# Performance work log

Measured on AMD Instinct MI355X. Metric: run time of the kernel, lower is better.

## Reference

```python
import jax, jax.numpy as jnp
import numpy as np

N = 100000
E = 1600000
IN_DIM = 1024
H_DIM = 16
DIM2 = H_DIM * 8  # 128


def _xavier(key, shape):
    fan_in, fan_out = shape[-2], shape[-1]
    lim = (6.0 / (fan_in + fan_out)) ** 0.5
    return jax.random.uniform(key, shape, jnp.float32, -lim, lim)


def setup_inputs() -> dict:
    key = jax.random.key(0)
    ks = jax.random.split(key, 10)
    x = jax.random.normal(ks[0], (N, IN_DIM), jnp.float32)
    edge_index = jax.random.randint(ks[1], (2, E), 0, N)
    perm = jax.random.permutation(ks[2], N)
    W1 = _xavier(ks[3], (IN_DIM, DIM2)); b1 = jnp.zeros((DIM2,), jnp.float32)
    W2 = _xavier(ks[4], (DIM2, DIM2)); b2 = jnp.zeros((DIM2,), jnp.float32)
    W3 = _xavier(ks[5], (DIM2, H_DIM)); b3 = jnp.zeros((H_DIM,), jnp.float32)
    Wdo = _xavier(ks[6], (1, DIM2, DIM2)); bdo = jnp.zeros((1,), jnp.float32)
    Wdh = _xavier(ks[7], (1, H_DIM, H_DIM)); bdh = jnp.zeros((1,), jnp.float32)
    return dict(x=x, W1=W1, b1=b1, W2=W2, b2=b2, W3=W3, b3=b3,
                Wdo=Wdo, bdo=bdo, Wdh=Wdh, bdh=bdh,
                edge_index=edge_index, perm=perm)


def _graph_conv(x, W, b, src, dst, norm_src, norm_dst):
    # DGL GraphConv, norm='both': D_dst^{-1/2} A D_src^{-1/2} X W + b
    h = (x * norm_src[:, None]) @ W          # mult W first (in >= out)
    agg = jax.ops.segment_sum(h[src], dst, num_segments=N)
    return agg * norm_dst[:, None] + b


def _l2norm(x):
    n = jnp.sqrt(jnp.sum(x * x, axis=1, keepdims=True))
    return x / jnp.maximum(n, 1e-12)


def _bilinear(a, c, W, b):
    # nn.Bilinear(n_h, n_h, 1): out[n,k] = a[n] @ W[k] @ c[n] + b[k]
    return jnp.einsum('nd,kde,ne->nk', a, W, c) + b


def reference(x, W1, b1, W2, b2, W3, b3, Wdo, bdo, Wdh, bdh, edge_index, perm):
    src, dst = edge_index[0], edge_index[1]
    ones = jnp.ones((E,), jnp.float32)
    deg_out = jnp.maximum(jax.ops.segment_sum(ones, src, num_segments=N), 1.0)
    deg_in = jnp.maximum(jax.ops.segment_sum(ones, dst, num_segments=N), 1.0)
    ns, nd = deg_out ** -0.5, deg_in ** -0.5

    def encode(xin):
        o = _graph_conv(xin, W1, b1, src, dst, ns, nd)
        o = _graph_conv(o, W2, b2, src, dst, ns, nd) + o
        h = _graph_conv(o, W3, b3, src, dst, ns, nd)
        emb_o = jax.nn.relu(o)
        g_o = jax.nn.sigmoid(_l2norm(emb_o))
        emb_h = jax.nn.relu(h)
        g_h = jax.nn.sigmoid(_l2norm(emb_h))
        return h, emb_o, g_o, emb_h, g_h

    h, emb_o, g_o, emb_h, g_h = encode(x)
    h_a, emb_oa, g_oa, emb_ha, g_ha = encode(x[perm])

    def disc(c, h_pl, h_mi, W, b):
        return jnp.concatenate([_bilinear(h_pl, c, W, b), _bilinear(h_mi, c, W, b)], axis=1)

    ret_o = disc(g_o, emb_o, emb_oa, Wdo, bdo)
    ret_oa = disc(g_oa, emb_oa, emb_o, Wdo, bdo)
    ret_h = disc(g_h, emb_h, emb_ha, Wdh, bdh)
    ret_ha = disc(g_ha, emb_ha, emb_h, Wdh, bdh)
    return (h, ret_o, ret_h, ret_oa, ret_ha)
```

## Files before the change

kernel.cpp:

```cpp
#include <hip/hip_runtime.h>
#include <math.h>

#define NN 100000
#define EE 1600000
#define SCB 98

typedef __attribute__((ext_vector_type(8))) short bf16x8;
typedef __attribute__((ext_vector_type(4))) short bf16x4;
typedef __attribute__((ext_vector_type(4))) float f32x4;

__device__ __forceinline__ unsigned short f2bf(float x){
  union { float f; unsigned u; } v; v.f = x;
  unsigned r = v.u + 0x7FFFu + ((v.u >> 16) & 1u);
  return (unsigned short)(r >> 16);
}
__device__ __forceinline__ float bf2f(unsigned short h){
  union { unsigned u; float f; } v; v.u = ((unsigned)h) << 16; return v.f;
}
__device__ __forceinline__ float sigm(float x){ return 1.0f/(1.0f+__expf(-x)); }

__device__ __forceinline__ void gload16(const unsigned short* g, unsigned short* l){
  __builtin_amdgcn_global_load_lds(
    (const __attribute__((address_space(1))) void*)g,
    (__attribute__((address_space(3))) void*)l, 16, 0, 0);
}
template<int N>
__device__ __forceinline__ void waitvm(){
  if constexpr (N==0) asm volatile("s_waitcnt vmcnt(0)" ::: "memory");
  else if constexpr (N==2) asm volatile("s_waitcnt vmcnt(2)" ::: "memory");
  else if constexpr (N==4) asm volatile("s_waitcnt vmcnt(4)" ::: "memory");
  else if constexpr (N==8) asm volatile("s_waitcnt vmcnt(8)" ::: "memory");
}
__device__ __forceinline__ void membar(){ asm volatile("" ::: "memory"); }

__global__ __launch_bounds__(256) void k_deg_wcvt(const int* __restrict__ src, const int* __restrict__ dst,
                      int* __restrict__ dout, int* __restrict__ din,
                      const float* __restrict__ W1, const float* __restrict__ W2,
                      const float* __restrict__ Wdo, const float* __restrict__ W3,
                      unsigned short* __restrict__ W1T, unsigned short* __restrict__ W2T,
                      unsigned short* __restrict__ WdoB, unsigned short* __restrict__ W3c){
  int b = blockIdx.x;
  if (b < EE/256){
    int e = b*256 + threadIdx.x;
    atomicAdd(&dout[src[e]],1); atomicAdd(&din[dst[e]],1);
  } else {
    int i = (b - EE/256)*256 + threadIdx.x;
    if (i < 131072){
      int c = i>>13, s = i&8191;
      int col = s>>6, p = (s>>3)&7, e2 = s&7;
      int k = c*64 + 8*(p ^ (col&7)) + e2;
      W1T[i] = f2bf(W1[(size_t)k*128 + col]);
    } else if (i < 147456){
      int j = i-131072;
      int c = j>>13, s = j&8191;
      int col = s>>6, p = (s>>3)&7, e2 = s&7;
      int k = c*64 + 8*(p ^ (col&7)) + e2;
      W2T[j] = f2bf(W2[(size_t)k*128 + col]);
    } else if (i < 163840){
      int j = i-147456;
      int c = j>>13, s = j&8191;
      int col = s>>6, p = (s>>3)&7, e2 = s&7;
      int k = c*64 + 8*(p ^ (col&7)) + e2;
      WdoB[j] = f2bf(Wdo[(size_t)col*128 + k]);
    } else if (i < 165888){
      int j = i-163840;
      int col = j>>7, k = j&127;
      W3c[j] = f2bf(W3[(size_t)k*16 + col]);
    }
  }
}

__global__ __launch_bounds__(1024) void k_scan1(const int* __restrict__ din, int* __restrict__ chunk,
                        int* __restrict__ bsum){
  __shared__ int wsum[16];
  int t = threadIdx.x, lane = t & 63, w = t >> 6;
  int i = blockIdx.x*1024 + t;
  int v = (i < NN) ? din[i] : 0;
  int x = v;
  #pragma unroll
  for (int off=1; off<64; off<<=1){
    int y = __shfl_up(x, off);
    if (lane>=off) x += y;
  }
  if (lane==63) wsum[w] = x;
  __syncthreads();
  int pre = 0;
  #pragma unroll
  for (int j=0;j<16;j++) if (j<w) pre += wsum[j];
  int incl = x + pre;
  if (i < NN) chunk[i] = incl;
  if (t == 1023) bsum[blockIdx.x] = incl;
}

__global__ __launch_bounds__(128) void k_scan2(const int* __restrict__ bsum, int* __restrict__ bpre,
                       int* __restrict__ row_ptr){
  __shared__ int w0tot;
  int t = threadIdx.x, lane = t & 63, w = t >> 6;
  int v = (t < SCB) ? bsum[t] : 0;
  int x = v;
  #pragma unroll
  for (int off=1; off<64; off<<=1){
    int y = __shfl_up(x, off);
    if (lane>=off) x += y;
  }
  if (w==0 && lane==63) w0tot = x;
  __syncthreads();
  int incl = x + (w ? w0tot : 0);
  if (t < SCB) bpre[t] = incl - v;
  if (t == 0) row_ptr[0] = 0;
}

__global__ __launch_bounds__(256) void k_scan3(const int* __restrict__ din, const int* __restrict__ chunk,
                       const int* __restrict__ bpre, const int* __restrict__ dout,
                       const int* __restrict__ perm,
                       int* __restrict__ row_ptr, int* __restrict__ cursor,
                       float* __restrict__ ns, float* __restrict__ nd, int* __restrict__ inv){
  int i = blockIdx.x*256 + threadIdx.x;
  if (i < NN){
    int d = din[i];
    int val = chunk[i] + bpre[i>>10];
    row_ptr[i+1] = val;
    cursor[i] = val - d;
    ns[i] = rsqrtf((float)max(dout[i],1));
    nd[i] = rsqrtf((float)max(d,1));
    inv[perm[i]] = i;
  }
}

__global__ __launch_bounds__(256) void k_fill(const int* __restrict__ src, const int* __restrict__ dst,
                       int* __restrict__ cursor, int* __restrict__ col){
  int e = blockIdx.x*256+threadIdx.x;
  if (e<EE){ int pos = atomicAdd(&cursor[dst[e]],1); col[pos] = src[e]; }
}

struct ARF { float4 a, b; };
struct ARU { bf16x8 a; };
__device__ __forceinline__ void aload(ARF& r, const float* p){
  r.a = *(const float4*)p; r.b = *(const float4*)(p+4);
}
__device__ __forceinline__ void aload(ARU& r, const unsigned short* p){
  r.a = *(const bf16x8*)p;
}
template<int IM>
__device__ __forceinline__ bf16x8 aconv(const ARF& r, float rs){
  float av[8] = {r.a.x,r.a.y,r.a.z,r.a.w,r.b.x,r.b.y,r.b.z,r.b.w};
  if constexpr (IM==1){
    #pragma unroll
    for (int i=0;i<8;i++) av[i] = sigm(fmaxf(av[i],0.0f)*rs);
  }
  bf16x8 o;
  #pragma unroll
  for (int i=0;i<8;i++) o[i] = (short)f2bf(av[i]);
  return o;
}
template<int IM>
__device__ __forceinline__ bf16x8 aconv(const ARU& r, float rs){
  if constexpr (IM==0) return r.a;
  else {
    bf16x8 o;
    #pragma unroll
    for (int i=0;i<8;i++){
      float v = sigm(fmaxf(bf2f((unsigned short)r.a[i]),0.0f)*rs);
      o[i] = (short)f2bf(v);
    }
    return o;
  }
}
__device__ __forceinline__ bf16x8 araw(const ARU& r){ return r.a; }
__device__ __forceinline__ bf16x8 araw(const ARF& r){
  bf16x8 o;
  float av[8] = {r.a.x,r.a.y,r.a.z,r.a.w,r.b.x,r.b.y,r.b.z,r.b.w};
  #pragma unroll
  for (int i=0;i<8;i++) o[i] = (short)f2bf(av[i]);
  return o;
}
template<typename T> struct ARofT;
template<> struct ARofT<float>{ using type = ARF; };
template<> struct ARofT<unsigned short>{ using type = ARU; };

template<int KDIM, int IN_MODE, int OUT_MODE, typename AT>
__global__ __launch_bounds__(256,4) void k_gemmA(
    const AT* __restrict__ A, const unsigned short* __restrict__ Wc,
    unsigned short* __restrict__ out0,
    const float* __restrict__ scale, const int* __restrict__ inv,
    const float* __restrict__ rn, int nrows,
    float* __restrict__ ro, float* __restrict__ roa,
    const unsigned short* __restrict__ W3c, const float* __restrict__ ns2,
    unsigned short* __restrict__ th)
{
  constexpr int NC = KDIM/64;
  constexpr int APC = (sizeof(AT)==4) ? 4 : 2;
  constexpr int BSSZ = 2*128*64 + (OUT_MODE==3 ? 2048 : 0);
  __shared__ __align__(16) unsigned short Bs[BSSZ];
  unsigned short* W3s = &Bs[16384];
  int t = threadIdx.x, wave = t>>6, lane = t&63;
  int row0 = blockIdx.x*64;
  int arow = row0 + wave*16 + (lane&15);
  int kof = (lane>>4)*8;
  int arow_c = min(arow, nrows-1);
  const AT* ap = A + (size_t)arow_c*KDIM + kof;
  float rscale = 1.0f;
  if constexpr (IN_MODE==1) rscale = rn[arow_c];

  unsigned short* b0 = &Bs[0];
  unsigned short* b1 = &Bs[128*64];
  const unsigned short* bcur = b0; unsigned short* bnxt = b1;

  f32x4 acc[8] = {};
  f32x4 acc2 = {};
  typename ARofT<AT>::type A0a{},A0b{},A1a{},A1b{},A2a{},A2b{};

  if constexpr (OUT_MODE==3){
    int wc = t>>4, wsl = t&15;
    bf16x8 v = *(const bf16x8*)(W3c + wc*128 + wsl*8);
    *(bf16x8*)&W3s[wc*128 + ((wsl ^ (wc&7))<<3)] = v;
  }
  membar();
  {
    unsigned short* lb = b0 + wave*2048;
    const unsigned short* gb = Wc + wave*2048 + lane*8;
    #pragma unroll
    for (int q=0;q<4;q++) gload16(gb + q*512, lb + q*512);
  }
  membar();
  aload(A0a, ap); aload(A0b, ap+32);
  if (NC>1){ aload(A1a, ap+64); aload(A1b, ap+96); }
  waitvm<2*APC>();
  asm volatile("s_waitcnt lgkmcnt(0)" ::: "memory");
  __builtin_amdgcn_s_barrier();
  __builtin_amdgcn_sched_barrier(0);

  int slot0 = lane>>4;
  int c = lane & 15;
  #pragma unroll
  for (int cc=0; cc<NC; ++cc){
    if (cc+1 < NC){
      unsigned short* lb = bnxt + wave*2048;
      const unsigned short* gb = Wc + (size_t)(cc+1)*8192 + wave*2048 + lane*8;
      #pragma unroll
      for (int q=0;q<4;q++) gload16(gb + q*512, lb + q*512);
    }
    membar();
    if (cc+2 < NC){
      aload(A2a, ap + (cc+2)*64);
      aload(A2b, ap + (cc+2)*64 + 32);
    }
    membar();
    {
      bf16x8 af = aconv<IN_MODE>(A0a, rscale);
      #pragma unroll
      for (int j=0;j<8;j++){
        int cj = j*16 + c;
        bf16x8 b = *(const bf16x8*)&bcur[cj*64 + ((slot0 ^ (cj&7))<<3)];
        acc[j] = __builtin_amdgcn_mfma_f32_16x16x32_bf16(af, b, acc[j], 0, 0, 0);
      }
      if constexpr (OUT_MODE==3){
        int sl = cc*8 + slot0;
        bf16x8 b = *(const bf16x8*)&W3s[c*128 + ((sl ^ (c&7))<<3)];
        acc2 = __builtin_amdgcn_mfma_f32_16x16x32_bf16(araw(A0a), b, acc2, 0, 0, 0);
      }
    }
    {
      bf16x8 af = aconv<IN_MODE>(A0b, rscale);
      #pragma unroll
      for (int j=0;j<8;j++){
        int cj = j*16 + c;
        bf16x8 b = *(const bf16x8*)&bcur[cj*64 + (((slot0+4) ^ (cj&7))<<3)];
        acc[j] = __builtin_amdgcn_mfma_f32_16x16x32_bf16(af, b, acc[j], 0, 0, 0);
      }
      if constexpr (OUT_MODE==3){
        int sl = cc*8 + 4 + slot0;
        bf16x8 b = *(const bf16x8*)&W3s[c*128 + ((sl ^ (c&7))<<3)];
        acc2 = __builtin_amdgcn_mfma_f32_16x16x32_bf16(araw(A0b), b, acc2, 0, 0, 0);
      }
    }
    if (cc+1 < NC){
      if (cc+2 < NC) waitvm<APC>(); else waitvm<0>();
      __builtin_amdgcn_s_barrier();
      __builtin_amdgcn_sched_barrier(0);
      const unsigned short* tmp = bcur; bcur = bnxt; bnxt = (unsigned short*)tmp;
    }
    A0a=A1a; A0b=A1b; A1a=A2a; A1b=A2b;
  }

  if constexpr (OUT_MODE==3){
    #pragma unroll
    for (int r=0;r<4;r++){
      int row = row0 + wave*16 + (lane>>4)*4 + r;
      int sidx = row>=NN ? row-NN : row;
      float v = acc2[r]*ns2[sidx];
      size_t tof = row<NN ? (size_t)row*32 + c : (size_t)(row-NN)*32 + 16 + c;
      th[tof] = f2bf(v);
    }
    __syncthreads();
    unsigned short* Os = &Bs[0];
    unsigned short* Oo = &Bs[8192];
    for (int p=t; p<2048; p+=256){
      int r = (p>>4)&63, seg = p&15;
      int row = row0 + r;
      int srcrow = (p<1024) ? row : (row<NN ? row+NN : row-NN);
      unsigned short* dst = (p<1024) ? Os : Oo;
      *(bf16x8*)&dst[r*128 + ((seg ^ (r&7))<<3)] = *(const bf16x8*)&A[(size_t)srcrow*128 + seg*8];
    }
    __syncthreads();
    float bb = scale[0];
    #pragma unroll
    for (int r=0;r<4;r++){
      int lr = wave*16 + (lane>>4)*4 + r;
      float dsame=0.f, doth=0.f;
      #pragma unroll
      for (int j=0;j<8;j++){
        float v = acc[j][r];
        int colj = j*16 + c;
        int idx = lr*128 + (((colj>>3) ^ (lr&7))<<3) + (colj&7);
        dsame += fmaxf(bf2f(Os[idx]),0.f)*v;
        doth  += fmaxf(bf2f(Oo[idx]),0.f)*v;
      }
      #pragma unroll
      for (int off=1; off<16; off<<=1){
        dsame += __shfl_xor(dsame, off);
        doth  += __shfl_xor(doth, off);
      }
      if (c==0){
        int row = row0 + lr;
        if (row < NN){
          ro[(size_t)row*2+0] = dsame + bb;
          ro[(size_t)row*2+1] = doth + bb;
        } else {
          int m = row - NN;
          roa[(size_t)m*2+0] = dsame + bb;
          roa[(size_t)m*2+1] = doth + bb;
        }
      }
    }
  } else {
    int rbase = row0 + wave*16 + (lane>>4)*4;
    #pragma unroll
    for (int j=0;j<8;j++){
      int colx = j*16 + c;
      #pragma unroll
      for (int r=0;r<4;r++){
        int row = rbase + r;
        if (row < nrows){
          float v = acc[j][r];
          if constexpr (OUT_MODE==0){
            out0[(size_t)row*256 + colx] = f2bf(v * scale[row]);
            int ir = inv[row];
            out0[(size_t)ir*256 + 128 + colx] = f2bf(v * scale[ir]);
          } else {
            int sidx = row >= NN ? row - NN : row;
            size_t zof = row < NN ? (size_t)row*256 + colx : (size_t)(row-NN)*256 + 128 + colx;
            out0[zof] = f2bf(v * scale[sidx]);
          }
        }
      }
    }
  }
}

template<bool RESID>
__global__ __launch_bounds__(256) void k_agg128(
  const unsigned short* __restrict__ z,
  const int* __restrict__ row_ptr, const int* __restrict__ col,
  const float* __restrict__ nd, const float* __restrict__ bias,
  unsigned short* __restrict__ ob, float* __restrict__ rn)
{
  int wave = threadIdx.x>>6, lane = threadIdx.x&63;
  int row = blockIdx.x*4 + wave;
  if (row >= NN) return;
  int s = row_ptr[row], e = row_ptr[row+1];
  int es = lane>>5;
  int half = (lane>>4)&1;
  int c8 = (lane&15)*8;
  size_t lof = (size_t)half*128 + c8;
  float acc[8] = {};
  int i = s + es;
  int c0 = (i < e) ? col[i] : -1;
  int c1 = (i+2 < e) ? col[i+2] : -1;
  bf16x8 u0 = {}, u1 = {};
  if (c0 >= 0) u0 = *(const bf16x8*)(z + (size_t)c0*256 + lof);
  if (c1 >= 0) u1 = *(const bf16x8*)(z + (size_t)c1*256 + lof);
  int d0 = (i+4 < e) ? col[i+4] : -1;
  int d1 = (i+6 < e) ? col[i+6] : -1;
  bf16x8 v0 = {}, v1 = {};
  if (d0 >= 0) v0 = *(const bf16x8*)(z + (size_t)d0*256 + lof);
  if (d1 >= 0) v1 = *(const bf16x8*)(z + (size_t)d1*256 + lof);
  while (c0 >= 0){
    int n0 = (i+8 < e) ? col[i+8] : -1;
    int n1 = (i+10 < e) ? col[i+10] : -1;
    bf16x8 w0 = {}, w1 = {};
    if (n0 >= 0) w0 = *(const bf16x8*)(z + (size_t)n0*256 + lof);
    if (n1 >= 0) w1 = *(const bf16x8*)(z + (size_t)n1*256 + lof);
    #pragma unroll
    for (int j=0;j<8;j++) acc[j] += bf2f((unsigned short)u0[j]);
    if (c1 >= 0){
      #pragma unroll
      for (int j=0;j<8;j++) acc[j] += bf2f((unsigned short)u1[j]);
    }
    c0=d0; c1=d1; u0=v0; u1=v1;
    d0=n0; d1=n1; v0=w0; v1=w1;
    i += 4;
  }
  #pragma unroll
  for (int j=0;j<8;j++) acc[j] += __shfl_down(acc[j], 32);
  if (lane < 32){
    float ndr = nd[row];
    size_t oof = half ? (size_t)(NN+row)*128 + c8 : (size_t)row*128 + c8;
    float ra[8];
    #pragma unroll
    for (int j=0;j<8;j++) ra[j] = acc[j]*ndr + bias[c8+j];
    if constexpr (RESID){
      bf16x8 pv = *(const bf16x8*)(ob + oof);
      #pragma unroll
      for (int j=0;j<8;j++) ra[j] += bf2f((unsigned short)pv[j]);
    }
    bf16x8 wv;
    #pragma unroll
    for (int j=0;j<8;j++) wv[j] = (short)f2bf(ra[j]);
    *(bf16x8*)(ob + oof) = wv;
    if constexpr (RESID){
      float sa = 0.f;
      #pragma unroll
      for (int j=0;j<8;j++){ float x1 = fmaxf(ra[j],0.f); sa += x1*x1; }
      sa += __shfl_down(sa, 8);
      sa += __shfl_down(sa, 4);
      sa += __shfl_down(sa, 2);
      sa += __shfl_down(sa, 1);
      if ((lane&15)==0) rn[half ? NN+row : row] = 1.0f/fmaxf(sqrtf(sa),1e-12f);
    }
  }
}

__global__ __launch_bounds__(256) void k_agg16(
  const unsigned short* __restrict__ th,
  const int* __restrict__ row_ptr, const int* __restrict__ col,
  const float* __restrict__ nd, const float* __restrict__ b3,
  const float* __restrict__ Wdh, const float* __restrict__ bdh,
  float* __restrict__ hout, float* __restrict__ rh, float* __restrict__ rha)
{
  __shared__ float Ws[256];
  __shared__ float hbuf[4][32];
  __shared__ float gbuf[4][32];
  int t = threadIdx.x;
  Ws[t] = Wdh[t];
  __syncthreads();
  int wave = t>>6, lane = t&63;
  int row = blockIdx.x*4 + wave;
  if (row >= NN) return;
  int s = row_ptr[row], e = row_ptr[row+1];
  int es = lane>>3, l8 = lane&7;
  float a4[4] = {};
  int i = s + es;
  int sc0 = (i<e)? col[i] : -1;
  int sc1 = (i+8<e)? col[i+8] : -1;
  bf16x4 u0 = {}, u1 = {};
  if (sc0 >= 0) u0 = *(const bf16x4*)(th + (size_t)sc0*32 + l8*4);
  if (sc1 >= 0) u1 = *(const bf16x4*)(th + (size_t)sc1*32 + l8*4);
  while (sc0 >= 0){
    int ni = i + 16;
    int nsc0 = (ni<e)? col[ni] : -1;
    int nsc1 = (ni+8<e)? col[ni+8] : -1;
    bf16x4 v0 = {}, v1 = {};
    if (nsc0 >= 0) v0 = *(const bf16x4*)(th + (size_t)nsc0*32 + l8*4);
    if (nsc1 >= 0) v1 = *(const bf16x4*)(th + (size_t)nsc1*32 + l8*4);
    #pragma unroll
    for (int j=0;j<4;j++) a4[j] += bf2f((unsigned short)u0[j]);
    if (sc1 >= 0){
      #pragma unroll
      for (int j=0;j<4;j++) a4[j] += bf2f((unsigned short)u1[j]);
    }
    u0 = v0; u1 = v1; sc0 = nsc0; sc1 = nsc1; i = ni;
  }
  #pragma unroll
  for (int j=0;j<4;j++){
    a4[j] += __shfl_down(a4[j], 32);
    a4[j] += __shfl_down(a4[j], 16);
    a4[j] += __shfl_down(a4[j], 8);
  }
  if (lane < 8){
    float ndr = nd[row];
    int half = l8>>2, c0 = (l8&3)*4;
    float4 r;
    r.x = a4[0]*ndr + b3[c0+0];
    r.y = a4[1]*ndr + b3[c0+1];
    r.z = a4[2]*ndr + b3[c0+2];
    r.w = a4[3]*ndr + b3[c0+3];
    if (half==0) *(float4*)&hout[(size_t)row*16 + c0] = r;
    int hb = half*16 + c0;
    hbuf[wave][hb+0]=r.x; hbuf[wave][hb+1]=r.y; hbuf[wave][hb+2]=r.z; hbuf[wave][hb+3]=r.w;
  }
  if (lane < 16){
    int d = lane;
    float e1v = fmaxf(hbuf[wave][d],    0.f);
    float e2v = fmaxf(hbuf[wave][16+d], 0.f);
    float s1 = e1v*e1v, s2 = e2v*e2v;
    #pragma unroll
    for (int off=1; off<16; off<<=1){
      s1 += __shfl_xor(s1, off);
      s2 += __shfl_xor(s2, off);
    }
    float r1 = 1.0f/fmaxf(sqrtf(s1),1e-12f);
    float r2 = 1.0f/fmaxf(sqrtf(s2),1e-12f);
    gbuf[wave][d]    = sigm(e1v*r1);
    gbuf[wave][16+d] = sigm(e2v*r2);
    float vh1=0.f, vh2=0.f;
    #pragma unroll
    for (int e2i=0;e2i<16;e2i++){
      float w = Ws[d*16+e2i];
      vh1 += w*gbuf[wave][e2i];
      vh2 += w*gbuf[wave][16+e2i];
    }
    float q00 = e1v*vh1, q01 = e2v*vh1, q10 = e2v*vh2, q11 = e1v*vh2;
    #pragma unroll
    for (int off=1; off<16; off<<=1){
      q00 += __shfl_xor(q00, off);
      q01 += __shfl_xor(q01, off);
      q10 += __shfl_xor(q10, off);
      q11 += __shfl_xor(q11, off);
    }
    if (lane==0){
      float bb = bdh[0];
      rh [(size_t)row*2+0]=q00+bb; rh [(size_t)row*2+1]=q01+bb;
      rha[(size_t)row*2+0]=q10+bb; rha[(size_t)row*2+1]=q11+bb;
    }
  }
}

extern "C" void kernel_launch(void* const* d_in, const int* in_sizes, int n_in,
                              void* d_out, int out_size, void* d_ws, size_t ws_size,
                              hipStream_t stream){
  const float* x   = (const float*)d_in[0];
  const float* W1  = (const float*)d_in[1];
  const float* b1  = (const float*)d_in[2];
  const float* W2  = (const float*)d_in[3];
  const float* b2  = (const float*)d_in[4];
  const float* W3  = (const float*)d_in[5];
  const float* b3  = (const float*)d_in[6];
  const float* Wdo = (const float*)d_in[7];
  const float* bdo = (const float*)d_in[8];
  const float* Wdh = (const float*)d_in[9];
  const float* bdh = (const float*)d_in[10];
  const int* ei    = (const int*)d_in[11];
  const int* perm  = (const int*)d_in[12];
  const int* esrc = ei;
  const int* edst = ei + EE;

  char* ws = (char*)d_ws;
  size_t off = 0;
  auto alloc = [&](size_t bytes)->void*{ void* p = ws + off; off += (bytes + 255) & ~(size_t)255; return p; };
  unsigned short* z  = (unsigned short*)alloc((size_t)NN*256*2);
  unsigned short* ob = (unsigned short*)alloc((size_t)2*NN*128*2);
  unsigned short* th = (unsigned short*)alloc((size_t)NN*32*2);
  int* deg = (int*)alloc((size_t)2*NN*4);
  int* dout_ = deg; int* din_ = deg + NN;
  float* ns = (float*)alloc((size_t)NN*4);
  float* nd = (float*)alloc((size_t)NN*4);
  int* inv  = (int*)alloc((size_t)NN*4);
  float* rn = (float*)alloc((size_t)2*NN*4);
  int* cursor = (int*)alloc((size_t)NN*4);
  int* row_ptr = (int*)alloc((size_t)(NN+1)*4);
  int* colx = (int*)alloc((size_t)EE*4);
  int* chunk = (int*)alloc((size_t)NN*4);
  int* bsum = (int*)alloc((size_t)SCB*4);
  int* bpre = (int*)alloc((size_t)SCB*4);
  unsigned short* W1T = (unsigned short*)alloc((size_t)1024*128*2);
  unsigned short* W2T = (unsigned short*)alloc((size_t)128*128*2);
  unsigned short* WdoB = (unsigned short*)alloc((size_t)128*128*2);
  unsigned short* W3c = (unsigned short*)alloc((size_t)16*128*2);

  float* out_h   = (float*)d_out;
  float* out_ro  = out_h  + (size_t)NN*16;
  float* out_rh  = out_ro + (size_t)NN*2;
  float* out_roa = out_rh + (size_t)NN*2;
  float* out_rha = out_roa+ (size_t)NN*2;

  hipMemsetAsync(deg, 0, (size_t)2*NN*4, stream);
  k_deg_wcvt<<<EE/256 + 648, 256, 0, stream>>>(esrc, edst, dout_, din_,
                                               W1, W2, Wdo, W3, W1T, W2T, WdoB, W3c);
  k_scan1<<<SCB, 1024, 0, stream>>>(din_, chunk, bsum);
  k_scan2<<<1, 128, 0, stream>>>(bsum, bpre, row_ptr);
  k_scan3<<<(NN+255)/256, 256, 0, stream>>>(din_, chunk, bpre, dout_, perm, row_ptr, cursor, ns, nd, inv);
  k_fill<<<EE/256, 256, 0, stream>>>(esrc, edst, cursor, colx);

  int gb1 = (NN + 63)/64;
  int gb2 = (2*NN)/64;
  k_gemmA<1024,0,0,float><<<gb1,256,0,stream>>>(x, W1T, z, ns, inv, nullptr, NN,
                                                nullptr, nullptr, nullptr, nullptr, nullptr);
  k_agg128<false><<<(NN+3)/4,256,0,stream>>>(z, row_ptr, colx, nd, b1, ob, nullptr);
  k_gemmA<128,0,1,unsigned short><<<gb2,256,0,stream>>>(ob, W2T, z, ns, nullptr, nullptr, 2*NN,
                                                nullptr, nullptr, nullptr, nullptr, nullptr);
  k_agg128<true><<<(NN+3)/4,256,0,stream>>>(z, row_ptr, colx, nd, b2, ob, rn);
  k_gemmA<128,1,3,unsigned short><<<gb2,256,0,stream>>>(ob, WdoB, nullptr, bdo, nullptr, rn, 2*NN,
                                                out_ro, out_roa, W3c, ns, th);
  k_agg16<<<(NN+3)/4,256,0,stream>>>(th, row_ptr, colx, nd, b3, Wdh, bdh, out_h, out_rh, out_rha);
}
```

Baseline: 761.2 us.

## Read GEMM weight fragments directly from global memory instead of staging in LDS

Removes the double-buffered LDS staging of weight tiles (global_load_lds, vmcnt waits, barriers) in the dense GEMM kernels. Each lane now loads its B fragments straight from a plain column-major bf16 weight copy, and the weight conversion drops the swizzle layout. This cuts barrier and LDS traffic at the cost of repeated global/L2 reads of the weights per block. The epilogue LDS buffer is kept only for the discriminator mode, and one __syncthreads before reusing shared memory is dropped, which is safe now that the buffer is no longer shared with the main loop.

Measured after the change: 997.6 us. 1.31x slower.

```diff
diff --git a/kernel.cpp b/kernel.cpp
--- a/kernel.cpp
+++ b/kernel.cpp
@@ -18,20 +18,6 @@
   union { unsigned u; float f; } v; v.u = ((unsigned)h) << 16; return v.f;
 }
 __device__ __forceinline__ float sigm(float x){ return 1.0f/(1.0f+__expf(-x)); }
-
-__device__ __forceinline__ void gload16(const unsigned short* g, unsigned short* l){
-  __builtin_amdgcn_global_load_lds(
-    (const __attribute__((address_space(1))) void*)g,
-    (__attribute__((address_space(3))) void*)l, 16, 0, 0);
-}
-template<int N>
-__device__ __forceinline__ void waitvm(){
-  if constexpr (N==0) asm volatile("s_waitcnt vmcnt(0)" ::: "memory");
-  else if constexpr (N==2) asm volatile("s_waitcnt vmcnt(2)" ::: "memory");
-  else if constexpr (N==4) asm volatile("s_waitcnt vmcnt(4)" ::: "memory");
-  else if constexpr (N==8) asm volatile("s_waitcnt vmcnt(8)" ::: "memory");
-}
-__device__ __forceinline__ void membar(){ asm volatile("" ::: "memory"); }
 
 __global__ __launch_bounds__(256) void k_deg_wcvt(const int* __restrict__ src, const int* __restrict__ dst,
                       int* __restrict__ dout, int* __restrict__ din,
@@ -46,22 +32,15 @@
   } else {
     int i = (b - EE/256)*256 + threadIdx.x;
     if (i < 131072){
-      int c = i>>13, s = i&8191;
-      int col = s>>6, p = (s>>3)&7, e2 = s&7;
-      int k = c*64 + 8*(p ^ (col&7)) + e2;
+      int col = i>>10, k = i&1023;
       W1T[i] = f2bf(W1[(size_t)k*128 + col]);
     } else if (i < 147456){
       int j = i-131072;
-      int c = j>>13, s = j&8191;
-      int col = s>>6, p = (s>>3)&7, e2 = s&7;
-      int k = c*64 + 8*(p ^ (col&7)) + e2;
+      int col = j>>7, k = j&127;
       W2T[j] = f2bf(W2[(size_t)k*128 + col]);
     } else if (i < 163840){
       int j = i-147456;
-      int c = j>>13, s = j&8191;
-      int col = s>>6, p = (s>>3)&7, e2 = s&7;
-      int k = c*64 + 8*(p ^ (col&7)) + e2;
-      WdoB[j] = f2bf(Wdo[(size_t)col*128 + k]);
+      WdoB[j] = f2bf(Wdo[j]);
     } else if (i < 165888){
       int j = i-163840;
       int col = j>>7, k = j&127;
@@ -179,7 +158,7 @@
 template<> struct ARofT<unsigned short>{ using type = ARU; };
 
 template<int KDIM, int IN_MODE, int OUT_MODE, typename AT>
-__global__ __launch_bounds__(256,4) void k_gemmA(
+__global__ __launch_bounds__(256,4) void k_gemmB(
     const AT* __restrict__ A, const unsigned short* __restrict__ Wc,
     unsigned short* __restrict__ out0,
     const float* __restrict__ scale, const int* __restrict__ inv,
@@ -189,10 +168,7 @@
     unsigned short* __restrict__ th)
 {
   constexpr int NC = KDIM/64;
-  constexpr int APC = (sizeof(AT)==4) ? 4 : 2;
-  constexpr int BSSZ = 2*128*64 + (OUT_MODE==3 ? 2048 : 0);
-  __shared__ __align__(16) unsigned short Bs[BSSZ];
-  unsigned short* W3s = &Bs[16384];
+  __shared__ __align__(16) unsigned short Es[OUT_MODE==3 ? 16384 : 8];
   int t = threadIdx.x, wave = t>>6, lane = t&63;
   int row0 = blockIdx.x*64;
   int arow = row0 + wave*16 + (lane&15);
@@ -202,61 +178,32 @@
   float rscale = 1.0f;
   if constexpr (IN_MODE==1) rscale = rn[arow_c];
 
-  unsigned short* b0 = &Bs[0];
-  unsigned short* b1 = &Bs[128*64];
-  const unsigned short* bcur = b0; unsigned short* bnxt = b1;
+  int c = lane & 15;
+  const unsigned short* bp = Wc + (size_t)c*KDIM + kof;
+  const unsigned short* w3p = W3c + (size_t)c*128 + kof;
 
   f32x4 acc[8] = {};
   f32x4 acc2 = {};
   typename ARofT<AT>::type A0a{},A0b{},A1a{},A1b{},A2a{},A2b{};
 
-  if constexpr (OUT_MODE==3){
-    int wc = t>>4, wsl = t&15;
-    bf16x8 v = *(const bf16x8*)(W3c + wc*128 + wsl*8);
-    *(bf16x8*)&W3s[wc*128 + ((wsl ^ (wc&7))<<3)] = v;
-  }
-  membar();
-  {
-    unsigned short* lb = b0 + wave*2048;
-    const unsigned short* gb = Wc + wave*2048 + lane*8;
-    #pragma unroll
-    for (int q=0;q<4;q++) gload16(gb + q*512, lb + q*512);
-  }
-  membar();
   aload(A0a, ap); aload(A0b, ap+32);
   if (NC>1){ aload(A1a, ap+64); aload(A1b, ap+96); }
-  waitvm<2*APC>();
-  asm volatile("s_waitcnt lgkmcnt(0)" ::: "memory");
-  __builtin_amdgcn_s_barrier();
-  __builtin_amdgcn_sched_barrier(0);
-
-  int slot0 = lane>>4;
-  int c = lane & 15;
+
   #pragma unroll
   for (int cc=0; cc<NC; ++cc){
-    if (cc+1 < NC){
-      unsigned short* lb = bnxt + wave*2048;
-      const unsigned short* gb = Wc + (size_t)(cc+1)*8192 + wave*2048 + lane*8;
-      #pragma unroll
-      for (int q=0;q<4;q++) gload16(gb + q*512, lb + q*512);
-    }
-    membar();
     if (cc+2 < NC){
       aload(A2a, ap + (cc+2)*64);
       aload(A2b, ap + (cc+2)*64 + 32);
     }
-    membar();
     {
       bf16x8 af = aconv<IN_MODE>(A0a, rscale);
       #pragma unroll
       for (int j=0;j<8;j++){
-        int cj = j*16 + c;
-        bf16x8 b = *(const bf16x8*)&bcur[cj*64 + ((slot0 ^ (cj&7))<<3)];
+        bf16x8 b = *(const bf16x8*)(bp + (size_t)j*16*KDIM + cc*64);
         acc[j] = __builtin_amdgcn_mfma_f32_16x16x32_bf16(af, b, acc[j], 0, 0, 0);
       }
       if constexpr (OUT_MODE==3){
-        int sl = cc*8 + slot0;
-        bf16x8 b = *(const bf16x8*)&W3s[c*128 + ((sl ^ (c&7))<<3)];
+        bf16x8 b = *(const bf16x8*)(w3p + cc*64);
         acc2 = __builtin_amdgcn_mfma_f32_16x16x32_bf16(araw(A0a), b, acc2, 0, 0, 0);
       }
     }
@@ -264,21 +211,13 @@
       bf16x8 af = aconv<IN_MODE>(A0b, rscale);
       #pragma unroll
       for (int j=0;j<8;j++){
-        int cj = j*16 + c;
-        bf16x8 b = *(const bf16x8*)&bcur[cj*64 + (((slot0+4) ^ (cj&7))<<3)];
+        bf16x8 b = *(const bf16x8*)(bp + (size_t)j*16*KDIM + cc*64 + 32);
         acc[j] = __builtin_amdgcn_mfma_f32_16x16x32_bf16(af, b, acc[j], 0, 0, 0);
       }
       if constexpr (OUT_MODE==3){
-        int sl = cc*8 + 4 + slot0;
-        bf16x8 b = *(const bf16x8*)&W3s[c*128 + ((sl ^ (c&7))<<3)];
+        bf16x8 b = *(const bf16x8*)(w3p + cc*64 + 32);
         acc2 = __builtin_amdgcn_mfma_f32_16x16x32_bf16(araw(A0b), b, acc2, 0, 0, 0);
       }
-    }
-    if (cc+1 < NC){
-      if (cc+2 < NC) waitvm<APC>(); else waitvm<0>();
-      __builtin_amdgcn_s_barrier();
-      __builtin_amdgcn_sched_barrier(0);
-      const unsigned short* tmp = bcur; bcur = bnxt; bnxt = (unsigned short*)tmp;
     }
     A0a=A1a; A0b=A1b; A1a=A2a; A1b=A2b;
   }
@@ -292,9 +231,8 @@
       size_t tof = row<NN ? (size_t)row*32 + c : (size_t)(row-NN)*32 + 16 + c;
       th[tof] = f2bf(v);
     }
-    __syncthreads();
-    unsigned short* Os = &Bs[0];
-    unsigned short* Oo = &Bs[8192];
+    unsigned short* Os = &Es[0];
+    unsigned short* Oo = &Es[8192];
     for (int p=t; p<2048; p+=256){
       int r = (p>>4)&63, seg = p&15;
       int row = row0 + r;
@@ -584,13 +522,13 @@
 
   int gb1 = (NN + 63)/64;
   int gb2 = (2*NN)/64;
-  k_gemmA<1024,0,0,float><<<gb1,256,0,stream>>>(x, W1T, z, ns, inv, nullptr, NN,
+  k_gemmB<1024,0,0,float><<<gb1,256,0,stream>>>(x, W1T, z, ns, inv, nullptr, NN,
                                                 nullptr, nullptr, nullptr, nullptr, nullptr);
   k_agg128<false><<<(NN+3)/4,256,0,stream>>>(z, row_ptr, colx, nd, b1, ob, nullptr);
-  k_gemmA<128,0,1,unsigned short><<<gb2,256,0,stream>>>(ob, W2T, z, ns, nullptr, nullptr, 2*NN,
+  k_gemmB<128,0,1,unsigned short><<<gb2,256,0,stream>>>(ob, W2T, z, ns, nullptr, nullptr, 2*NN,
                                                 nullptr, nullptr, nullptr, nullptr, nullptr);
   k_agg128<true><<<(NN+3)/4,256,0,stream>>>(z, row_ptr, colx, nd, b2, ob, rn);
-  k_gemmA<128,1,3,unsigned short><<<gb2,256,0,stream>>>(ob, WdoB, nullptr, bdo, nullptr, rn, 2*NN,
+  k_gemmB<128,1,3,unsigned short><<<gb2,256,0,stream>>>(ob, WdoB, nullptr, bdo, nullptr, rn, 2*NN,
                                                 out_ro, out_roa, W3c, ns, th);
   k_agg16<<<(NN+3)/4,256,0,stream>>>(th, row_ptr, colx, nd, b3, Wdh, bdh, out_h, out_rh, out_rha);
 }
```

## Stage GEMM operands through registers into LDS with coalesced A tiles

Applied to the files above, without the earlier changes.

Adds a dedicated first-layer GEMM kernel that loads the fp32 input in coalesced row-major chunks, converts it to bf16 and writes it to a padded LDS tile, double-buffered alongside the weights. The weight staging in all GEMMs switches from direct global-to-LDS loads to register loads followed by swizzled LDS stores, and the weight pre-layout drops its swizzle. The aim is better coalescing of the large 1024-wide input read and overlap of global loads with MFMA work, at the cost of extra LDS traffic, more registers and an extra barrier per chunk.

Result: no change. 760.5 us (-0.1%).

```diff
diff --git a/kernel.cpp b/kernel.cpp
--- a/kernel.cpp
+++ b/kernel.cpp
@@ -19,19 +19,11 @@
 }
 __device__ __forceinline__ float sigm(float x){ return 1.0f/(1.0f+__expf(-x)); }
 
-__device__ __forceinline__ void gload16(const unsigned short* g, unsigned short* l){
-  __builtin_amdgcn_global_load_lds(
-    (const __attribute__((address_space(1))) void*)g,
-    (__attribute__((address_space(3))) void*)l, 16, 0, 0);
-}
-template<int N>
-__device__ __forceinline__ void waitvm(){
-  if constexpr (N==0) asm volatile("s_waitcnt vmcnt(0)" ::: "memory");
-  else if constexpr (N==2) asm volatile("s_waitcnt vmcnt(2)" ::: "memory");
-  else if constexpr (N==4) asm volatile("s_waitcnt vmcnt(4)" ::: "memory");
-  else if constexpr (N==8) asm volatile("s_waitcnt vmcnt(8)" ::: "memory");
-}
-__device__ __forceinline__ void membar(){ asm volatile("" ::: "memory"); }
+__device__ __forceinline__ void barrier_lds_only(){
+  asm volatile("s_waitcnt lgkmcnt(0)" ::: "memory");
+  __builtin_amdgcn_s_barrier();
+  __builtin_amdgcn_sched_barrier(0);
+}
 
 __global__ __launch_bounds__(256) void k_deg_wcvt(const int* __restrict__ src, const int* __restrict__ dst,
                       int* __restrict__ dout, int* __restrict__ din,
@@ -46,21 +38,15 @@
   } else {
     int i = (b - EE/256)*256 + threadIdx.x;
     if (i < 131072){
-      int c = i>>13, s = i&8191;
-      int col = s>>6, p = (s>>3)&7, e2 = s&7;
-      int k = c*64 + 8*(p ^ (col&7)) + e2;
+      int c = i>>13, r = i&8191, col = r>>6, k = c*64 + (r&63);
       W1T[i] = f2bf(W1[(size_t)k*128 + col]);
     } else if (i < 147456){
       int j = i-131072;
-      int c = j>>13, s = j&8191;
-      int col = s>>6, p = (s>>3)&7, e2 = s&7;
-      int k = c*64 + 8*(p ^ (col&7)) + e2;
+      int c = j>>13, r = j&8191, col = r>>6, k = c*64 + (r&63);
       W2T[j] = f2bf(W2[(size_t)k*128 + col]);
     } else if (i < 163840){
       int j = i-147456;
-      int c = j>>13, s = j&8191;
-      int col = s>>6, p = (s>>3)&7, e2 = s&7;
-      int k = c*64 + 8*(p ^ (col&7)) + e2;
+      int c = j>>13, r = j&8191, col = r>>6, k = c*64 + (r&63);
       WdoB[j] = f2bf(Wdo[(size_t)col*128 + k]);
     } else if (i < 165888){
       int j = i-163840;
@@ -133,25 +119,123 @@
   if (e<EE){ int pos = atomicAdd(&cursor[dst[e]],1); col[pos] = src[e]; }
 }
 
-struct ARF { float4 a, b; };
+__global__ __launch_bounds__(256,4) void k_gemm1(
+    const float* __restrict__ A, const unsigned short* __restrict__ Wc,
+    unsigned short* __restrict__ z, const float* __restrict__ ns,
+    const int* __restrict__ inv)
+{
+  constexpr int NC = 16;
+  __shared__ __align__(16) unsigned short As[2*64*72];
+  __shared__ __align__(16) unsigned short Bs[2*128*64];
+  int t = threadIdx.x, wave = t>>6, lane = t&63;
+  int row0 = blockIdx.x*64;
+
+  int srow = t>>4;
+  int scol4 = (t&15)*4;
+  int scolB = t>>3;
+  int swB = ((t&7) ^ (scolB&7))<<3;
+
+  f32x4 acc[8] = {};
+  float4 Ar0[4], Ar1[4];
+  bf16x8 w0{},w1{},w2{},w3{};
+
+#define ALOAD(SET, CC) { \
+  _Pragma("unroll") \
+  for (int p=0;p<4;p++){ \
+    int rr = min(row0 + p*16 + srow, NN-1); \
+    SET[p] = *(const float4*)(A + (size_t)rr*1024 + (CC)*64 + scol4); } }
+
+#define AWRITE(SET, BUF) { \
+  _Pragma("unroll") \
+  for (int p=0;p<4;p++){ \
+    short4 s4; \
+    s4.x = (short)f2bf(SET[p].x); s4.y = (short)f2bf(SET[p].y); \
+    s4.z = (short)f2bf(SET[p].z); s4.w = (short)f2bf(SET[p].w); \
+    *(short4*)&As[(BUF)*4608 + (p*16+srow)*72 + scol4] = s4; } }
+
+#define BLOAD(CC) { \
+  const unsigned short* gp = Wc + (size_t)(CC)*8192 + (size_t)t*8; \
+  w0 = *(const bf16x8*)(gp); \
+  w1 = *(const bf16x8*)(gp+2048); \
+  w2 = *(const bf16x8*)(gp+4096); \
+  w3 = *(const bf16x8*)(gp+6144); }
+
+#define BWRITE(BUF) { \
+  unsigned short* bb = &Bs[(BUF)*8192]; \
+  *(bf16x8*)&bb[(0*32+scolB)*64 + swB] = w0; \
+  *(bf16x8*)&bb[(1*32+scolB)*64 + swB] = w1; \
+  *(bf16x8*)&bb[(2*32+scolB)*64 + swB] = w2; \
+  *(bf16x8*)&bb[(3*32+scolB)*64 + swB] = w3; }
+
+  ALOAD(Ar0, 0);
+  BLOAD(0);
+  BWRITE(0);
+  AWRITE(Ar0, 0);
+  ALOAD(Ar1, 1);
+  BLOAD(1);
+  barrier_lds_only();
+
+  int slot0 = lane>>4;
+  int c = lane & 15;
+  int arow = wave*16 + (lane&15);
+  #pragma unroll
+  for (int cc=0; cc<NC; ++cc){
+    if (cc+2 < NC){
+      if (cc&1) { ALOAD(Ar1, cc+2); } else { ALOAD(Ar0, cc+2); }
+    }
+    int cur = cc&1;
+    const unsigned short* ab = &As[cur*4608];
+    const unsigned short* bb = &Bs[cur*8192];
+    {
+      bf16x8 af = *(const bf16x8*)&ab[arow*72 + (slot0<<3)];
+      #pragma unroll
+      for (int j=0;j<8;j++){
+        int cj = j*16 + c;
+        bf16x8 b = *(const bf16x8*)&bb[cj*64 + ((slot0 ^ (cj&7))<<3)];
+        acc[j] = __builtin_amdgcn_mfma_f32_16x16x32_bf16(af, b, acc[j], 0, 0, 0);
+      }
+    }
+    {
+      bf16x8 af = *(const bf16x8*)&ab[arow*72 + 32 + (slot0<<3)];
+      #pragma unroll
+      for (int j=0;j<8;j++){
+        int cj = j*16 + c;
+        bf16x8 b = *(const bf16x8*)&bb[cj*64 + (((slot0+4) ^ (cj&7))<<3)];
+        acc[j] = __builtin_amdgcn_mfma_f32_16x16x32_bf16(af, b, acc[j], 0, 0, 0);
+      }
+    }
+    if (cc+1 < NC){
+      if (cc&1) { AWRITE(Ar0, (cc+1)&1); } else { AWRITE(Ar1, (cc+1)&1); }
+      BWRITE((cc+1)&1);
+      barrier_lds_only();
+      if (cc+2 < NC) BLOAD(cc+2);
+    }
+  }
+#undef ALOAD
+#undef AWRITE
+#undef BLOAD
+#undef BWRITE
+
+  int rbase = row0 + wave*16 + (lane>>4)*4;
+  #pragma unroll
+  for (int j=0;j<8;j++){
+    int colx = j*16 + c;
+    #pragma unroll
+    for (int r=0;r<4;r++){
+      int row = rbase + r;
+      if (row < NN){
+        float v = acc[j][r];
+        z[(size_t)row*256 + colx] = f2bf(v * ns[row]);
+        int ir = inv[row];
+        z[(size_t)ir*256 + 128 + colx] = f2bf(v * ns[ir]);
+      }
+    }
+  }
+}
+
 struct ARU { bf16x8 a; };
-__device__ __forceinline__ void aload(ARF& r, const float* p){
-  r.a = *(const float4*)p; r.b = *(const float4*)(p+4);
-}
 __device__ __forceinline__ void aload(ARU& r, const unsigned short* p){
   r.a = *(const bf16x8*)p;
-}
-template<int IM>
-__device__ __forceinline__ bf16x8 aconv(const ARF& r, float rs){
-  float av[8] = {r.a.x,r.a.y,r.a.z,r.a.w,r.b.x,r.b.y,r.b.z,r.b.w};
-  if constexpr (IM==1){
-    #pragma unroll
-    for (int i=0;i<8;i++) av[i] = sigm(fmaxf(av[i],0.0f)*rs);
-  }
-  bf16x8 o;
-  #pragma unroll
-  for (int i=0;i<8;i++) o[i] = (short)f2bf(av[i]);
-  return o;
 }
 template<int IM>
 __device__ __forceinline__ bf16x8 aconv(const ARU& r, float rs){
@@ -167,40 +251,31 @@
   }
 }
 __device__ __forceinline__ bf16x8 araw(const ARU& r){ return r.a; }
-__device__ __forceinline__ bf16x8 araw(const ARF& r){
-  bf16x8 o;
-  float av[8] = {r.a.x,r.a.y,r.a.z,r.a.w,r.b.x,r.b.y,r.b.z,r.b.w};
-  #pragma unroll
-  for (int i=0;i<8;i++) o[i] = (short)f2bf(av[i]);
-  return o;
-}
-template<typename T> struct ARofT;
-template<> struct ARofT<float>{ using type = ARF; };
-template<> struct ARofT<unsigned short>{ using type = ARU; };
-
-template<int KDIM, int IN_MODE, int OUT_MODE, typename AT>
+
+template<int KDIM, int IN_MODE, int OUT_MODE>
 __global__ __launch_bounds__(256,4) void k_gemmA(
-    const AT* __restrict__ A, const unsigned short* __restrict__ Wc,
+    const unsigned short* __restrict__ A, const unsigned short* __restrict__ Wc,
     unsigned short* __restrict__ out0,
-    const float* __restrict__ scale, const int* __restrict__ inv,
+    const float* __restrict__ scale,
     const float* __restrict__ rn, int nrows,
     float* __restrict__ ro, float* __restrict__ roa,
     const unsigned short* __restrict__ W3c, const float* __restrict__ ns2,
     unsigned short* __restrict__ th)
 {
   constexpr int NC = KDIM/64;
-  constexpr int APC = (sizeof(AT)==4) ? 4 : 2;
-  constexpr int BSSZ = 2*128*64 + (OUT_MODE==3 ? 2048 : 0);
-  __shared__ __align__(16) unsigned short Bs[BSSZ];
-  unsigned short* W3s = &Bs[16384];
+  __shared__ __align__(16) unsigned short Bs[2*128*64];
+  __shared__ __align__(16) unsigned short W3s[OUT_MODE==3 ? 16*128 : 16];
   int t = threadIdx.x, wave = t>>6, lane = t&63;
   int row0 = blockIdx.x*64;
   int arow = row0 + wave*16 + (lane&15);
   int kof = (lane>>4)*8;
   int arow_c = min(arow, nrows-1);
-  const AT* ap = A + (size_t)arow_c*KDIM + kof;
+  const unsigned short* ap = A + (size_t)arow_c*KDIM + kof;
   float rscale = 1.0f;
   if constexpr (IN_MODE==1) rscale = rn[arow_c];
+
+  int scol = t>>3;
+  int sw = ((t&7) ^ (scol&7))<<3;
 
   unsigned short* b0 = &Bs[0];
   unsigned short* b1 = &Bs[128*64];
@@ -208,44 +283,44 @@
 
   f32x4 acc[8] = {};
   f32x4 acc2 = {};
-  typename ARofT<AT>::type A0a{},A0b{},A1a{},A1b{},A2a{},A2b{};
-
+  ARU A0a{},A0b{},A1a{},A1b{},A2a{},A2b{};
+  bf16x8 w0{},w1{},w2{},w3{};
+
+  {
+    const unsigned short* gp = Wc + (size_t)t*8;
+    bf16x8 t0 = *(const bf16x8*)(gp);
+    bf16x8 t1 = *(const bf16x8*)(gp+2048);
+    bf16x8 t2 = *(const bf16x8*)(gp+4096);
+    bf16x8 t3 = *(const bf16x8*)(gp+6144);
+    *(bf16x8*)&b0[(0*32+scol)*64 + sw] = t0;
+    *(bf16x8*)&b0[(1*32+scol)*64 + sw] = t1;
+    *(bf16x8*)&b0[(2*32+scol)*64 + sw] = t2;
+    *(bf16x8*)&b0[(3*32+scol)*64 + sw] = t3;
+  }
   if constexpr (OUT_MODE==3){
     int wc = t>>4, wsl = t&15;
     bf16x8 v = *(const bf16x8*)(W3c + wc*128 + wsl*8);
     *(bf16x8*)&W3s[wc*128 + ((wsl ^ (wc&7))<<3)] = v;
   }
-  membar();
-  {
-    unsigned short* lb = b0 + wave*2048;
-    const unsigned short* gb = Wc + wave*2048 + lane*8;
-    #pragma unroll
-    for (int q=0;q<4;q++) gload16(gb + q*512, lb + q*512);
-  }
-  membar();
   aload(A0a, ap); aload(A0b, ap+32);
-  if (NC>1){ aload(A1a, ap+64); aload(A1b, ap+96); }
-  waitvm<2*APC>();
-  asm volatile("s_waitcnt lgkmcnt(0)" ::: "memory");
-  __builtin_amdgcn_s_barrier();
-  __builtin_amdgcn_sched_barrier(0);
+  if (NC>1){
+    const unsigned short* gp = Wc + 8192 + (size_t)t*8;
+    w0 = *(const bf16x8*)(gp);
+    w1 = *(const bf16x8*)(gp+2048);
+    w2 = *(const bf16x8*)(gp+4096);
+    w3 = *(const bf16x8*)(gp+6144);
+    aload(A1a, ap+64); aload(A1b, ap+96);
+  }
+  __syncthreads();
 
   int slot0 = lane>>4;
   int c = lane & 15;
   #pragma unroll
   for (int cc=0; cc<NC; ++cc){
-    if (cc+1 < NC){
-      unsigned short* lb = bnxt + wave*2048;
-      const unsigned short* gb = Wc + (size_t)(cc+1)*8192 + wave*2048 + lane*8;
-      #pragma unroll
-      for (int q=0;q<4;q++) gload16(gb + q*512, lb + q*512);
-    }
-    membar();
     if (cc+2 < NC){
       aload(A2a, ap + (cc+2)*64);
       aload(A2b, ap + (cc+2)*64 + 32);
     }
-    membar();
     {
       bf16x8 af = aconv<IN_MODE>(A0a, rscale);
       #pragma unroll
@@ -275,10 +350,19 @@
       }
     }
     if (cc+1 < NC){
-      if (cc+2 < NC) waitvm<APC>(); else waitvm<0>();
-      __builtin_amdgcn_s_barrier();
-      __builtin_amdgcn_sched_barrier(0);
+      *(bf16x8*)&bnxt[(0*32+scol)*64 + sw] = w0;
+      *(bf16x8*)&bnxt[(1*32+scol)*64 + sw] = w1;
+      *(bf16x8*)&bnxt[(2*32+scol)*64 + sw] = w2;
+      *(bf16x8*)&bnxt[(3*32+scol)*64 + sw] = w3;
+      barrier_lds_only();
       const unsigned short* tmp = bcur; bcur = bnxt; bnxt = (unsigned short*)tmp;
+      if (cc+2 < NC){
+        const unsigned short* gp = Wc + (size_t)(cc+2)*8192 + (size_t)t*8;
+        w0 = *(const bf16x8*)(gp);
+        w1 = *(const bf16x8*)(gp+2048);
+        w2 = *(const bf16x8*)(gp+4096);
+        w3 = *(const bf16x8*)(gp+6144);
+      }
     }
     A0a=A1a; A0b=A1b; A1a=A2a; A1b=A2b;
   }
@@ -343,15 +427,9 @@
         int row = rbase + r;
         if (row < nrows){
           float v = acc[j][r];
-          if constexpr (OUT_MODE==0){
-            out0[(size_t)row*256 + colx] = f2bf(v * scale[row]);
-            int ir = inv[row];
-            out0[(size_t)ir*256 + 128 + colx] = f2bf(v * scale[ir]);
-          } else {
-            int sidx = row >= NN ? row - NN : row;
-            size_t zof = row < NN ? (size_t)row*256 + colx : (size_t)(row-NN)*256 + 128 + colx;
-            out0[zof] = f2bf(v * scale[sidx]);
-          }
+          int sidx = row >= NN ? row - NN : row;
+          size_t zof = row < NN ? (size_t)row*256 + colx : (size_t)(row-NN)*256 + 128 + colx;
+          out0[zof] = f2bf(v * scale[sidx]);
         }
       }
     }
@@ -584,13 +662,12 @@
 
   int gb1 = (NN + 63)/64;
   int gb2 = (2*NN)/64;
-  k_gemmA<1024,0,0,float><<<gb1,256,0,stream>>>(x, W1T, z, ns, inv, nullptr, NN,
-                                                nullptr, nullptr, nullptr, nullptr, nullptr);
+  k_gemm1<<<gb1,256,0,stream>>>(x, W1T, z, ns, inv);
   k_agg128<false><<<(NN+3)/4,256,0,stream>>>(z, row_ptr, colx, nd, b1, ob, nullptr);
-  k_gemmA<128,0,1,unsigned short><<<gb2,256,0,stream>>>(ob, W2T, z, ns, nullptr, nullptr, 2*NN,
-                                                nullptr, nullptr, nullptr, nullptr, nullptr);
+  k_gemmA<128,0,1><<<gb2,256,0,stream>>>(ob, W2T, z, ns, nullptr, 2*NN,
+                                         nullptr, nullptr, nullptr, nullptr, nullptr);
   k_agg128<true><<<(NN+3)/4,256,0,stream>>>(z, row_ptr, colx, nd, b2, ob, rn);
-  k_gemmA<128,1,3,unsigned short><<<gb2,256,0,stream>>>(ob, WdoB, nullptr, bdo, nullptr, rn, 2*NN,
-                                                out_ro, out_roa, W3c, ns, th);
+  k_gemmA<128,1,3><<<gb2,256,0,stream>>>(ob, WdoB, nullptr, bdo, rn, 2*NN,
+                                         out_ro, out_roa, W3c, ns, th);
   k_agg16<<<(NN+3)/4,256,0,stream>>>(th, row_ptr, colx, nd, b3, Wdh, bdh, out_h, out_rh, out_rha);
 }
```
